# Performance work log

Hardware: AMD Instinct MI355X
Metric: run time of the kernel (lower is better)

## Reference

```python
import jax, jax.numpy as jnp
import numpy as np
from jax import lax

BN_EPS = 1e-5
STRIDE = 1
PAD = 1  # autopad(3, d=1) = 1
DIL = 1
GROUPS = 1


def setup_inputs() -> dict:
    key = jax.random.key(0)
    ks = jax.random.split(key, 4)
    b, cin, h, w = 16, 256, 56, 56
    E, cout, k = 8, 256, 3
    x = jax.random.normal(ks[0], (b, cin, h, w), dtype=jnp.float32)
    routing_w = jax.random.normal(ks[1], (E, cin), dtype=jnp.float32) * (1.0 / np.sqrt(cin))
    routing_b = jax.random.normal(ks[2], (E,), dtype=jnp.float32) * 0.01
    # kaiming_normal fan_out: std = sqrt(2 / (cout * k * k))
    kw_std = np.sqrt(2.0 / (cout * k * k)).astype(np.float32)
    kernel_weights = jax.random.normal(ks[3], (E, cout, cin // GROUPS, k, k), dtype=jnp.float32) * kw_std
    bn_gamma = jnp.ones((cout,), dtype=jnp.float32)
    bn_beta = jnp.zeros((cout,), dtype=jnp.float32)
    bn_mean = jnp.zeros((cout,), dtype=jnp.float32)
    bn_var = jnp.ones((cout,), dtype=jnp.float32)
    return {"x": x, "routing_w": routing_w, "routing_b": routing_b,
            "kernel_weights": kernel_weights, "bn_gamma": bn_gamma,
            "bn_beta": bn_beta, "bn_mean": bn_mean, "bn_var": bn_var}


def reference(x, routing_w, routing_b, kernel_weights, bn_gamma, bn_beta, bn_mean, bn_var):
    # Routing: sigmoid(Linear(GAP(x)))  -> (b, E)
    pooled = x.mean(axis=(2, 3))                                   # (b, cin)
    r = jax.nn.sigmoid(pooled @ routing_w.T + routing_b)           # (b, E)
    # Per-sample combined kernels: sum_e r[b,e] * W[e]  -> (b, cout, cin, k, k)
    cw = jnp.einsum('be,eoihw->boihw', r, kernel_weights)
    # Per-sample conv (equivalent to the grouped conv with groups=b trick)
    def conv1(xi, wi):
        # xi: (cin, H, W), wi: (cout, cin, k, k)
        return lax.conv_general_dilated(
            xi[None], wi,
            window_strides=(STRIDE, STRIDE),
            padding=((PAD, PAD), (PAD, PAD)),
            rhs_dilation=(DIL, DIL),
            dimension_numbers=('NCHW', 'OIHW', 'NCHW'),
            feature_group_count=GROUPS)[0]
    y = jax.vmap(conv1)(x, cw)                                     # (b, cout, H, W)
    # BatchNorm (inference form) + SiLU
    inv = bn_gamma / jnp.sqrt(bn_var + BN_EPS)
    y = y * inv[None, :, None, None] + (bn_beta - bn_mean * inv)[None, :, None, None]
    return jax.nn.silu(y)
```

## Files before the change

### kernel.cpp

```cpp
#include <hip/hip_runtime.h>
#include <hip/hip_bf16.h>

typedef unsigned short u16;
typedef __attribute__((ext_vector_type(8))) short s16x8;
typedef __attribute__((ext_vector_type(4))) float f32x4;
typedef __attribute__((address_space(3))) u16 lds_u16;
typedef __attribute__((address_space(1))) const u16 g_u16;

#define CIN 256
#define COUT 256
#define NPIX 3136
#define CWROW 168
#define CWPB (16 * COUT * CWROW)

__device__ __forceinline__ u16 f2b(float f) {
  union { float f; unsigned u; } c; c.f = f;
  unsigned r = (c.u + 0x7FFFu + ((c.u >> 16) & 1u)) >> 16;
  return (u16)r;
}

__global__ __launch_bounds__(256)
void transpose_gap_kernel(const float* __restrict__ x, u16* __restrict__ xq,
                          float* __restrict__ pooled) {
  const int hg = blockIdx.x, ck = blockIdx.y, b = blockIdx.z;
  const int tid = threadIdx.x;
  const int ci = tid >> 4, sub = tid & 15;
  __shared__ __align__(16) u16 tile[928 * 8];

  if (tid < 32) {
    int r = tid >> 2, c4 = tid & 3;
    int u = r * 116 + (c4 < 2 ? c4 : 112 + c4);
    int us = u ^ ((u >> 3) & 7);
    *(uint4*)&tile[us * 8] = (uint4){0, 0, 0, 0};
  }

  const float* src = x + ((size_t)(b * CIN + ck * 16 + ci) * NPIX + (size_t)hg * 448);
  float s = 0.f;
#pragma unroll
  for (int it = 0; it < 7; ++it) {
    int p = it * 16 + sub;
    int row = p / 14, wq = p - row * 14;
    float4 v = *(const float4*)(src + p * 4);
    s += v.x + v.y + v.z + v.w;
    u16 q[4] = { f2b(v.x), f2b(v.y), f2b(v.z), f2b(v.w) };
#pragma unroll
    for (int k = 0; k < 4; ++k) {
      int wp = wq * 4 + 1 + k;
      int u = (row * 58 + wp) * 2 + (ci >> 3);
      int us = u ^ ((u >> 3) & 7);
      tile[us * 8 + (ci & 7)] = q[k];
    }
  }
  for (int off = 8; off; off >>= 1) s += __shfl_down(s, off, 16);
  if (sub == 0) atomicAdd(&pooled[b * CIN + ck * 16 + ci], s);

  __syncthreads();
  uint4* dst = (uint4*)(xq + ((size_t)(b * 16 + ck) * 58 + hg * 8 + 1) * 928);
  for (int idx = tid; idx < 928; idx += 256) {
    int us = idx ^ ((idx >> 3) & 7);
    dst[idx] = *(const uint4*)&tile[us * 8];
  }
  if (hg == 0 && tid < 116)
    ((uint4*)(xq + ((size_t)(b * 16 + ck) * 58) * 928))[tid] = (uint4){0, 0, 0, 0};
  if (hg == 6 && tid < 116)
    ((uint4*)(xq + ((size_t)(b * 16 + ck) * 58 + 57) * 928))[tid] = (uint4){0, 0, 0, 0};
}

__global__ __launch_bounds__(256)
void combine_kernel(const float* __restrict__ W, const float* __restrict__ pooled,
                    const float* __restrict__ rw, const float* __restrict__ rb,
                    u16* __restrict__ cw) {
  const int o = blockIdx.x, tid = threadIdx.x;
  __shared__ float rs[128];
  __shared__ __align__(16) u16 st[2][16 * CWROW];

  for (int i = tid; i < 672; i += 256) ((uint4*)st)[i] = (uint4){0, 0, 0, 0};

  if (tid < 128) {
    int b = tid >> 3, e = tid & 7;
    float s = rb[e];
    const float* pb = pooled + b * CIN;
    const float* we = rw + e * CIN;
    for (int c = 0; c < CIN; ++c) s += (pb[c] * (1.f / 3136.f)) * we[c];
    rs[tid] = 1.f / (1.f + __expf(-s));
  }
  float wreg[8][9];
#pragma unroll
  for (int e = 0; e < 8; ++e) {
    const float* wp = W + ((size_t)(e * COUT + o)) * 2304 + tid;
#pragma unroll
    for (int k = 0; k < 9; ++k) wreg[e][k] = wp[k * 256];
  }
  int slot[9];
#pragma unroll
  for (int k = 0; k < 9; ++k) {
    int j = tid + k * 256, ci = j / 9, t = j - ci * 9;
    slot[k] = (ci >> 4) * CWROW + t * 16 + (ci & 15);
  }
  __syncthreads();
  for (int b = 0; b < 16; ++b) {
    u16* sb = st[b & 1];
    float rv[8];
#pragma unroll
    for (int e = 0; e < 8; ++e) rv[e] = rs[b * 8 + e];
#pragma unroll
    for (int k = 0; k < 9; ++k) {
      float a = 0.f;
#pragma unroll
      for (int e = 0; e < 8; ++e) a += rv[e] * wreg[e][k];
      sb[slot[k]] = f2b(a);
    }
    __syncthreads();
    u16* dstb = cw + (size_t)b * CWPB;
    for (int i = tid; i < 336; i += 256) {
      int ck = i / 21, q = i - ck * 21;
      *(uint4*)(dstb + ck * (256 * CWROW) + o * CWROW + q * 8) =
          *(const uint4*)(sb + ck * CWROW + q * 8);
    }
  }
}

__global__ __launch_bounds__(256)
void conv_kernel(const u16* __restrict__ xq, const u16* __restrict__ cw,
                 const float* __restrict__ bng, const float* __restrict__ bnb,
                 const float* __restrict__ bnm, const float* __restrict__ bnv,
                 float* __restrict__ out) {
  const int l = blockIdx.x;
  const int xcd = l & 7, s = l >> 3;
  const int bb = (s >= 28) ? 1 : 0;
  const int b = xcd + 8 * bb;
  const int r = s - 28 * bb;
  const int ob = r / 7;
  const int o0 = ob * 64, h0 = (r - ob * 7) * 8;
  const int tid = threadIdx.x;
  const int wv = tid >> 6, lane = tid & 63, quad = lane >> 4, ln = lane & 15;

  __shared__ __align__(16) u16 xs[2][19 * 512];
  __shared__ __align__(16) u16 as_[2][64 * CWROW];

  f32x4 acc[4][7];
#pragma unroll
  for (int ms = 0; ms < 4; ++ms)
#pragma unroll
    for (int ns = 0; ns < 7; ++ns) acc[ms][ns] = (f32x4){0.f, 0.f, 0.f, 0.f};

  int bsite[7];
#pragma unroll
  for (int ns = 0; ns < 7; ++ns) {
    int pi = ns * 16 + ln;
    int hr = (pi >= 56) ? 1 : 0;
    int wc = pi - hr * 56;
    bsite[ns] = ((2 * wv + hr) * 58 + wc) * 16;
  }

  auto STAGE = [&](int ck, int buf) {
    const u16* xsrc = xq + ((size_t)(b * 16 + ck) * 58 + h0) * 928;
    const u16* asrc = cw + (size_t)b * CWPB + ((size_t)ck * COUT + o0) * CWROW;
    for (int g = wv; g < 40; g += 4) {
      if (g < 19)
        __builtin_amdgcn_global_load_lds((g_u16*)(xsrc + g * 512 + lane * 8),
                                         (lds_u16*)(&xs[buf][g * 512]), 16, 0, 0);
      else
        __builtin_amdgcn_global_load_lds((g_u16*)(asrc + (g - 19) * 512 + lane * 8),
                                         (lds_u16*)(&as_[buf][(g - 19) * 512]), 16, 0, 0);
    }
  };

  auto COMPUTE = [&](int buf) {
#pragma unroll
    for (int tp = 0; tp < 5; ++tp) {
      int t = tp * 2 + (quad >> 1);
      int dy, dx;
      if (t < 9) { dy = t / 3; dx = t - dy * 3; } else { dy = 1; dx = 1; }
      const int boff = (dy * 58 + dx) * 16 + (quad & 1) * 8;
      s16x8 af[4];
#pragma unroll
      for (int ms = 0; ms < 4; ++ms)
        af[ms] = *(const s16x8*)&as_[buf][(ms * 16 + ln) * CWROW + tp * 32 + quad * 8];
#pragma unroll
      for (int ns = 0; ns < 7; ++ns) {
        s16x8 bfr = *(const s16x8*)&xs[buf][bsite[ns] + boff];
#pragma unroll
        for (int ms = 0; ms < 4; ++ms)
          acc[ms][ns] = __builtin_amdgcn_mfma_f32_16x16x32_bf16(af[ms], bfr, acc[ms][ns], 0, 0, 0);
      }
    }
  };

  STAGE(0, 0);
  __syncthreads();
  for (int ck = 0; ck < 16; ck += 2) {
    STAGE(ck + 1, 1);
    COMPUTE(0);
    __syncthreads();
    if (ck < 14) STAGE(ck + 2, 0);
    COMPUTE(1);
    __syncthreads();
  }

#pragma unroll
  for (int ms = 0; ms < 4; ++ms) {
#pragma unroll
    for (int rr = 0; rr < 4; ++rr) {
      int o = o0 + ms * 16 + quad * 4 + rr;
      float inv = bng[o] * rsqrtf(bnv[o] + 1e-5f);
      float bias = bnb[o] - bnm[o] * inv;
      float* obp = out + ((size_t)(b * COUT + o)) * NPIX;
#pragma unroll
      for (int ns = 0; ns < 7; ++ns) {
        int pi = ns * 16 + ln;
        int hr = (pi >= 56) ? 1 : 0;
        int wc = pi - hr * 56;
        int hg = h0 + 2 * wv + hr;
        float v = acc[ms][ns][rr] * inv + bias;
        v = v / (1.f + __expf(-v));
        obp[hg * 56 + wc] = v;
      }
    }
  }
}

extern "C" void kernel_launch(void* const* d_in, const int* in_sizes, int n_in,
                              void* d_out, int out_size, void* d_ws, size_t ws_size,
                              hipStream_t stream) {
  const float* x   = (const float*)d_in[0];
  const float* rw  = (const float*)d_in[1];
  const float* rb  = (const float*)d_in[2];
  const float* W   = (const float*)d_in[3];
  const float* bng = (const float*)d_in[4];
  const float* bnb = (const float*)d_in[5];
  const float* bnm = (const float*)d_in[6];
  const float* bnv = (const float*)d_in[7];
  float* out = (float*)d_out;

  char* wsb = (char*)d_ws;
  u16*  cw     = (u16*)wsb;
  u16*  xq     = (u16*)(wsb + 22020096);
  float* pooled = (float*)(wsb + 22020096 + 27558912);

  hipMemsetAsync(pooled, 0, 16 * CIN * sizeof(float), stream);
  transpose_gap_kernel<<<dim3(7, 16, 16), 256, 0, stream>>>(x, xq, pooled);
  combine_kernel<<<256, 256, 0, stream>>>(W, pooled, rw, rb, cw);
  conv_kernel<<<dim3(448), 256, 0, stream>>>(xq, cw, bng, bnb, bnm, bnv, out);
}
```

Measured before the change: 233.4 us.

## Fuse transpose, combine and conv into one cooperative kernel with grid syncs

Result: slower. 242.3 us (+3.8%).

```diff
diff --git a/kernel.cpp b/kernel.cpp
--- a/kernel.cpp
+++ b/kernel.cpp
@@ -1,5 +1,6 @@
 #include <hip/hip_runtime.h>
 #include <hip/hip_bf16.h>
+#include <hip/hip_cooperative_groups.h>
 
 typedef unsigned short u16;
 typedef __attribute__((ext_vector_type(8))) short s16x8;
@@ -19,21 +20,16 @@
   return (u16)r;
 }
 
-__global__ __launch_bounds__(256)
-void transpose_gap_kernel(const float* __restrict__ x, u16* __restrict__ xq,
-                          float* __restrict__ pooled) {
-  const int hg = blockIdx.x, ck = blockIdx.y, b = blockIdx.z;
-  const int tid = threadIdx.x;
+__device__ __forceinline__ void transpose_unit(int hg, int ck, int b,
+    const float* __restrict__ x, u16* __restrict__ xq, float* __restrict__ parts,
+    u16* tile , int tid) {
   const int ci = tid >> 4, sub = tid & 15;
-  __shared__ __align__(16) u16 tile[928 * 8];
-
   if (tid < 32) {
     int r = tid >> 2, c4 = tid & 3;
     int u = r * 116 + (c4 < 2 ? c4 : 112 + c4);
     int us = u ^ ((u >> 3) & 7);
     *(uint4*)&tile[us * 8] = (uint4){0, 0, 0, 0};
   }
-
   const float* src = x + ((size_t)(b * CIN + ck * 16 + ci) * NPIX + (size_t)hg * 448);
   float s = 0.f;
 #pragma unroll
@@ -52,8 +48,7 @@
     }
   }
   for (int off = 8; off; off >>= 1) s += __shfl_down(s, off, 16);
-  if (sub == 0) atomicAdd(&pooled[b * CIN + ck * 16 + ci], s);
-
+  if (sub == 0) parts[(hg * 16 + b) * 256 + ck * 16 + ci] = s;
   __syncthreads();
   uint4* dst = (uint4*)(xq + ((size_t)(b * 16 + ck) * 58 + hg * 8 + 1) * 928);
   for (int idx = tid; idx < 928; idx += 256) {
@@ -64,22 +59,28 @@
     ((uint4*)(xq + ((size_t)(b * 16 + ck) * 58) * 928))[tid] = (uint4){0, 0, 0, 0};
   if (hg == 6 && tid < 116)
     ((uint4*)(xq + ((size_t)(b * 16 + ck) * 58 + 57) * 928))[tid] = (uint4){0, 0, 0, 0};
-}
-
-__global__ __launch_bounds__(256)
-void combine_kernel(const float* __restrict__ W, const float* __restrict__ pooled,
-                    const float* __restrict__ rw, const float* __restrict__ rb,
-                    u16* __restrict__ cw) {
-  const int o = blockIdx.x, tid = threadIdx.x;
-  __shared__ float rs[128];
-  __shared__ __align__(16) u16 st[2][16 * CWROW];
-
-  for (int i = tid; i < 672; i += 256) ((uint4*)st)[i] = (uint4){0, 0, 0, 0};
-
+  __syncthreads();
+}
+
+__device__ __forceinline__ void combine_unit(int o, const float* __restrict__ W,
+    const float* __restrict__ parts, const float* __restrict__ rw,
+    const float* __restrict__ rb, u16* __restrict__ cw, char* smem, int tid) {
+  float* pooled_lds = (float*)smem;
+  float* rs = (float*)(smem + 16384);
+  u16* st = (u16*)(smem + 16896);
+  for (int b = 0; b < 16; ++b) {
+    float s = 0.f;
+#pragma unroll
+    for (int hg = 0; hg < 7; ++hg) s += parts[(hg * 16 + b) * 256 + tid];
+    pooled_lds[b * 256 + tid] = s;
+  }
+  for (int i = tid; i < (2 * 16 * CWROW) / 8; i += 256)
+    ((uint4*)st)[i] = (uint4){0, 0, 0, 0};
+  __syncthreads();
   if (tid < 128) {
     int b = tid >> 3, e = tid & 7;
     float s = rb[e];
-    const float* pb = pooled + b * CIN;
+    const float* pb = pooled_lds + b * 256;
     const float* we = rw + e * CIN;
     for (int c = 0; c < CIN; ++c) s += (pb[c] * (1.f / 3136.f)) * we[c];
     rs[tid] = 1.f / (1.f + __expf(-s));
@@ -99,7 +100,7 @@
   }
   __syncthreads();
   for (int b = 0; b < 16; ++b) {
-    u16* sb = st[b & 1];
+    u16* sb = st + (b & 1) * (16 * CWROW);
     float rv[8];
 #pragma unroll
     for (int e = 0; e < 8; ++e) rv[e] = rs[b * 8 + e];
@@ -120,23 +121,20 @@
   }
 }
 
-__global__ __launch_bounds__(256)
-void conv_kernel(const u16* __restrict__ xq, const u16* __restrict__ cw,
-                 const float* __restrict__ bng, const float* __restrict__ bnb,
-                 const float* __restrict__ bnm, const float* __restrict__ bnv,
-                 float* __restrict__ out) {
-  const int l = blockIdx.x;
+__device__ __forceinline__ void conv_unit(int l, const u16* __restrict__ xq,
+    const u16* __restrict__ cw, const float* __restrict__ bng, const float* __restrict__ bnb,
+    const float* __restrict__ bnm, const float* __restrict__ bnv, float* __restrict__ out,
+    char* smem, int tid) {
   const int xcd = l & 7, s = l >> 3;
   const int bb = (s >= 28) ? 1 : 0;
   const int b = xcd + 8 * bb;
   const int r = s - 28 * bb;
   const int ob = r / 7;
   const int o0 = ob * 64, h0 = (r - ob * 7) * 8;
-  const int tid = threadIdx.x;
   const int wv = tid >> 6, lane = tid & 63, quad = lane >> 4, ln = lane & 15;
 
-  __shared__ __align__(16) u16 xs[2][19 * 512];
-  __shared__ __align__(16) u16 as_[2][64 * CWROW];
+  u16* xsb[2] = { (u16*)smem,            (u16*)(smem + 18560) };
+  u16* asb[2] = { (u16*)(smem + 37120),  (u16*)(smem + 58624) };
 
   f32x4 acc[4][7];
 #pragma unroll
@@ -157,12 +155,16 @@
     const u16* xsrc = xq + ((size_t)(b * 16 + ck) * 58 + h0) * 928;
     const u16* asrc = cw + (size_t)b * CWPB + ((size_t)ck * COUT + o0) * CWROW;
     for (int g = wv; g < 40; g += 4) {
-      if (g < 19)
+      if (g < 18)
         __builtin_amdgcn_global_load_lds((g_u16*)(xsrc + g * 512 + lane * 8),
-                                         (lds_u16*)(&xs[buf][g * 512]), 16, 0, 0);
-      else
+                                         (lds_u16*)(xsb[buf] + g * 512), 16, 0, 0);
+      else if (g == 18) {
+        if (lane < 8)
+          __builtin_amdgcn_global_load_lds((g_u16*)(xsrc + 9216 + lane * 8),
+                                           (lds_u16*)(xsb[buf] + 9216), 16, 0, 0);
+      } else
         __builtin_amdgcn_global_load_lds((g_u16*)(asrc + (g - 19) * 512 + lane * 8),
-                                         (lds_u16*)(&as_[buf][(g - 19) * 512]), 16, 0, 0);
+                                         (lds_u16*)(asb[buf] + (g - 19) * 512), 16, 0, 0);
     }
   };
 
@@ -176,10 +178,10 @@
       s16x8 af[4];
 #pragma unroll
       for (int ms = 0; ms < 4; ++ms)
-        af[ms] = *(const s16x8*)&as_[buf][(ms * 16 + ln) * CWROW + tp * 32 + quad * 8];
+        af[ms] = *(const s16x8*)&asb[buf][(ms * 16 + ln) * CWROW + tp * 32 + quad * 8];
 #pragma unroll
       for (int ns = 0; ns < 7; ++ns) {
-        s16x8 bfr = *(const s16x8*)&xs[buf][bsite[ns] + boff];
+        s16x8 bfr = *(const s16x8*)&xsb[buf][bsite[ns] + boff];
 #pragma unroll
         for (int ms = 0; ms < 4; ++ms)
           acc[ms][ns] = __builtin_amdgcn_mfma_f32_16x16x32_bf16(af[ms], bfr, acc[ms][ns], 0, 0, 0);
@@ -218,6 +220,58 @@
       }
     }
   }
+}
+
+__global__ __launch_bounds__(256)
+void transpose_gap_kernel(const float* __restrict__ x, u16* __restrict__ xq,
+                          float* __restrict__ parts) {
+  __shared__ __align__(16) u16 tile[7424];
+  transpose_unit(blockIdx.x, blockIdx.y, blockIdx.z, x, xq, parts, tile, threadIdx.x);
+}
+
+__global__ __launch_bounds__(256)
+void combine_kernel(const float* __restrict__ W, const float* __restrict__ parts,
+                    const float* __restrict__ rw, const float* __restrict__ rb,
+                    u16* __restrict__ cw) {
+  __shared__ __align__(16) char smem[27648];
+  combine_unit(blockIdx.x, W, parts, rw, rb, cw, smem, threadIdx.x);
+}
+
+__global__ __launch_bounds__(256)
+void conv_kernel(const u16* __restrict__ xq, const u16* __restrict__ cw,
+                 const float* __restrict__ bng, const float* __restrict__ bnb,
+                 const float* __restrict__ bnm, const float* __restrict__ bnv,
+                 float* __restrict__ out) {
+  __shared__ __align__(16) char smem[80128];
+  conv_unit(blockIdx.x, xq, cw, bng, bnb, bnm, bnv, out, smem, threadIdx.x);
+}
+
+__global__ __launch_bounds__(256)
+void fused_kernel(const float* __restrict__ x, const float* __restrict__ rw,
+                  const float* __restrict__ rb, const float* __restrict__ W,
+                  const float* __restrict__ bng, const float* __restrict__ bnb,
+                  const float* __restrict__ bnm, const float* __restrict__ bnv,
+                  float* __restrict__ out, u16* __restrict__ cw, u16* __restrict__ xq,
+                  float* __restrict__ parts) {
+  __shared__ __align__(16) char smem[80128];
+  const int l = blockIdx.x, tid = threadIdx.x;
+  {
+    const int xcd = l & 7, s = l >> 3;
+    const int b = xcd + 8 * (s & 1);
+    const int base = (s >> 1) * 4;
+#pragma unroll
+    for (int i = 0; i < 4; ++i) {
+      int idx = base + i;
+      int hg = idx % 7, ck = idx / 7;
+      transpose_unit(hg, ck, b, x, xq, parts, (u16*)smem, tid);
+    }
+  }
+  __threadfence();
+  cooperative_groups::this_grid().sync();
+  if (l < 256) combine_unit(l, W, parts, rw, rb, cw, smem, tid);
+  __threadfence();
+  cooperative_groups::this_grid().sync();
+  conv_unit(l, xq, cw, bng, bnb, bnm, bnv, out, smem, tid);
 }
 
 extern "C" void kernel_launch(void* const* d_in, const int* in_sizes, int n_in,
@@ -234,12 +288,28 @@
   float* out = (float*)d_out;
 
   char* wsb = (char*)d_ws;
-  u16*  cw     = (u16*)wsb;
-  u16*  xq     = (u16*)(wsb + 22020096);
-  float* pooled = (float*)(wsb + 22020096 + 27558912);
-
-  hipMemsetAsync(pooled, 0, 16 * CIN * sizeof(float), stream);
-  transpose_gap_kernel<<<dim3(7, 16, 16), 256, 0, stream>>>(x, xq, pooled);
-  combine_kernel<<<256, 256, 0, stream>>>(W, pooled, rw, rb, cw);
-  conv_kernel<<<dim3(448), 256, 0, stream>>>(xq, cw, bng, bnb, bnm, bnv, out);
-}
+  u16*  cw    = (u16*)wsb;
+  u16*  xq    = (u16*)(wsb + 22020096);
+  float* parts = (float*)(wsb + 22020096 + 27558912);
+
+  static int coopBlocks = -1;
+  if (coopBlocks < 0) {
+    int mb = 0;
+    hipError_t e = hipOccupancyMaxActiveBlocksPerMultiprocessor(&mb, (const void*)fused_kernel,
+                                                                256, 0);
+    coopBlocks = (e == hipSuccess) ? mb : 0;
+  }
+  hipError_t le = hipErrorUnknown;
+  if (coopBlocks >= 2) {
+    void* args[12] = { (void*)&x, (void*)&rw, (void*)&rb, (void*)&W, (void*)&bng, (void*)&bnb,
+                       (void*)&bnm, (void*)&bnv, (void*)&out, (void*)&cw, (void*)&xq,
+                       (void*)&parts };
+    le = hipLaunchCooperativeKernel((const void*)fused_kernel, dim3(448), dim3(256),
+                                    args, 0u, stream);
+  }
+  if (le != hipSuccess) {
+    transpose_gap_kernel<<<dim3(7, 16, 16), 256, 0, stream>>>(x, xq, parts);
+    combine_kernel<<<256, 256, 0, stream>>>(W, parts, rw, rb, cw);
+    conv_kernel<<<dim3(448), 256, 0, stream>>>(xq, cw, bng, bnb, bnm, bnv, out);
+  }
+}
```
